# Optimization experiments

Hardware: AMD Instinct MI355X
Metric: run time of the kernel (lower is better)

Reference implementation:

```python
import jax, jax.numpy as jnp
import numpy as np

B, T, D, P, M = 4, 1024, 512, 64, 256


def setup_inputs() -> dict:
    key = jax.random.key(0)
    ks = jax.random.split(key, 10)
    s_d = 1.0 / np.sqrt(D)
    s_m = 1.0 / np.sqrt(M)
    s_p = 1.0 / np.sqrt(P)
    return {
        "inputs": jax.random.normal(ks[0], (B, T, D), dtype=jnp.float32),
        "ec": jax.random.normal(ks[1], (B, M), dtype=jnp.float32),
        "W1": jax.random.uniform(ks[2], (D, P), jnp.float32, -s_d, s_d),
        "b1": jax.random.uniform(ks[3], (P,), jnp.float32, -s_d, s_d),
        "W2": jax.random.uniform(ks[4], (D, P), jnp.float32, -s_d, s_d),
        "b2": jax.random.uniform(ks[5], (P,), jnp.float32, -s_d, s_d),
        "W3": jax.random.uniform(ks[6], (M, P), jnp.float32, -s_m, s_m),
        "b3": jax.random.uniform(ks[7], (P,), jnp.float32, -s_m, s_m),
        "wa_w": jax.random.uniform(ks[8], (P,), jnp.float32, -s_p, s_p),
        "wa_b": jax.random.uniform(ks[9], (), jnp.float32, -s_p, s_p),
    }


def reference(inputs, ec, W1, b1, W2, b2, W3, b3, wa_w, wa_b):
    # inputs: (B,T,D), ec: (B,M)
    w1h = inputs @ W1 + b1          # (B,T,P)
    w2h = inputs @ W2 + b2          # (B,T,P)
    w3e = ec @ W3 + b3              # (B,P)
    # Gt: (B,T,T,P) via broadcast add + tanh
    gt = jnp.tanh(w1h[:, :, None, :] + w2h[:, None, :, :] + w3e[:, None, None, :])
    at = jnp.einsum('btup,p->btu', gt, wa_w) + wa_b   # (B,T,T)
    at = jax.nn.softmax(at, axis=-1)
    out = jnp.einsum('btu,bud->btd', at, inputs)      # (B,T,D)
    return out
```

## Files before the change

kernel.cpp:

```cpp
#include <hip/hip_runtime.h>
#include <hip/hip_bf16.h>

constexpr int BB = 4;
constexpr int TT = 1024;
constexpr int DD = 512;
constexpr int PP = 64;
constexpr int MM = 256;

constexpr float CSCALE = 2.8853900817779268f;
constexpr float L2E = 1.4426950408889634f;

typedef __attribute__((ext_vector_type(8))) short v8s;
typedef __attribute__((ext_vector_type(4))) float v4f;

__device__ __forceinline__ unsigned short f2bf(float f) {
    unsigned u = __builtin_bit_cast(unsigned, f);
    unsigned r = (u + 0x7fffu + ((u >> 16) & 1u)) >> 16;
    return (unsigned short)r;
}

__global__ __launch_bounds__(256) void prep_kernel(
    const float* __restrict__ x, const float* __restrict__ ec,
    const float* __restrict__ W1, const float* __restrict__ b1,
    const float* __restrict__ W2, const float* __restrict__ b2,
    const float* __restrict__ W3, const float* __restrict__ b3,
    float* __restrict__ E1, float* __restrict__ E2, float* __restrict__ E3,
    unsigned short* __restrict__ xt) {
    __shared__ float tile[64][65];
    int bid = blockIdx.x;
    int tid = threadIdx.x;
    if (bid < 512) {
        int p = tid & 63;
        int rr = tid >> 6;
        int row0 = (bid << 3) + (rr << 1);
        const float* xr0 = x + (size_t)row0 * DD;
        const float* xr1 = xr0 + DD;
        float a10 = b1[p], a11 = b1[p];
        float a20 = b2[p], a21 = b2[p];
        #pragma unroll 4
        for (int d = 0; d < DD; d++) {
            float wv1 = W1[d * PP + p];
            float wv2 = W2[d * PP + p];
            float x0 = xr0[d];
            float x1 = xr1[d];
            a10 = fmaf(x0, wv1, a10);
            a11 = fmaf(x1, wv1, a11);
            a20 = fmaf(x0, wv2, a20);
            a21 = fmaf(x1, wv2, a21);
        }
        E1[(size_t)row0 * PP + p]       = __builtin_amdgcn_exp2f(a10 * CSCALE);
        E1[(size_t)(row0 + 1) * PP + p] = __builtin_amdgcn_exp2f(a11 * CSCALE);
        E2[(size_t)row0 * PP + p]       = __builtin_amdgcn_exp2f(a20 * CSCALE);
        E2[(size_t)(row0 + 1) * PP + p] = __builtin_amdgcn_exp2f(a21 * CSCALE);
    } else if (bid < 1024) {
        int q = bid - 512;
        int d0 = (q & 7) << 6;
        int u0 = ((q >> 3) & 15) << 6;
        int b = q >> 7;
        int c4 = (tid & 15) << 2, r = tid >> 4;
        #pragma unroll
        for (int i = 0; i < 4; i++) {
            int row = r + (i << 4);
            float4 v = *(const float4*)(x + ((size_t)b * TT + u0 + row) * DD + d0 + c4);
            tile[row][c4 + 0] = v.x;
            tile[row][c4 + 1] = v.y;
            tile[row][c4 + 2] = v.z;
            tile[row][c4 + 3] = v.w;
        }
        __syncthreads();
        int dd = tid >> 2;
        int uq = (tid & 3) << 4;
        unsigned short us[16];
        #pragma unroll
        for (int j = 0; j < 16; j++) us[j] = f2bf(tile[uq + j][dd]);
        uint4 w0, w1;
        w0.x = us[0] | ((unsigned)us[1] << 16);  w0.y = us[2] | ((unsigned)us[3] << 16);
        w0.z = us[4] | ((unsigned)us[5] << 16);  w0.w = us[6] | ((unsigned)us[7] << 16);
        w1.x = us[8] | ((unsigned)us[9] << 16);  w1.y = us[10] | ((unsigned)us[11] << 16);
        w1.z = us[12] | ((unsigned)us[13] << 16); w1.w = us[14] | ((unsigned)us[15] << 16);
        unsigned short* dst = xt + ((size_t)b * DD + d0 + dd) * TT + u0 + uq;
        *(uint4*)dst = w0;
        *(uint4*)(dst + 8) = w1;
    } else {
        int b = tid >> 6, p = tid & 63;
        float a = b3[p];
        const float* e = ec + (size_t)b * MM;
        #pragma unroll 4
        for (int m = 0; m < MM; m++) a = fmaf(e[m], W3[m * PP + p], a);
        E3[b * PP + p] = __builtin_amdgcn_exp2f(a * CSCALE);
    }
}

__global__ __launch_bounds__(256) void scores_kernel(
    const float* __restrict__ E1, const float* __restrict__ E2,
    const float* __restrict__ E3, const float* __restrict__ wa_w,
    const float* __restrict__ wa_b, unsigned short* __restrict__ at_bf) {
    __shared__ float sc_lds[32][256];
    __shared__ float sm[4][4];
    __shared__ float sl[4][4];
    int tid = threadIdx.x;
    int bid = blockIdx.x;
    int b = bid >> 8;
    int t0 = (bid & 255) << 2;
    int pp = tid & 7;
    int uu = tid >> 3;
    int p0 = pp << 3;
    int lane = tid & 63;
    int wv = tid >> 6;
    int my_i = pp & 3;

    float ww2[8], H[4][8];
    float base;
    {
        float4 wv0 = *(const float4*)(wa_w + p0);
        float4 wv1 = *(const float4*)(wa_w + p0 + 4);
        float s = wv0.x + wv0.y + wv0.z + wv0.w + wv1.x + wv1.y + wv1.z + wv1.w;
        s += __shfl_xor(s, 1, 64);
        s += __shfl_xor(s, 2, 64);
        s += __shfl_xor(s, 4, 64);
        base = (s + wa_b[0]) * L2E;
        ww2[0] = -2.f * L2E * wv0.x; ww2[1] = -2.f * L2E * wv0.y;
        ww2[2] = -2.f * L2E * wv0.z; ww2[3] = -2.f * L2E * wv0.w;
        ww2[4] = -2.f * L2E * wv1.x; ww2[5] = -2.f * L2E * wv1.y;
        ww2[6] = -2.f * L2E * wv1.z; ww2[7] = -2.f * L2E * wv1.w;
        float4 e3a = *(const float4*)(E3 + (b << 6) + p0);
        float4 e3b = *(const float4*)(E3 + (b << 6) + p0 + 4);
        #pragma unroll
        for (int i = 0; i < 4; i++) {
            const float* e1p = E1 + (((size_t)(b << 10) + t0 + i) << 6) + p0;
            float4 a = *(const float4*)e1p;
            float4 c = *(const float4*)(e1p + 4);
            H[i][0] = a.x * e3a.x; H[i][1] = a.y * e3a.y; H[i][2] = a.z * e3a.z; H[i][3] = a.w * e3a.w;
            H[i][4] = c.x * e3b.x; H[i][5] = c.y * e3b.y; H[i][6] = c.z * e3b.z; H[i][7] = c.w * e3b.w;
        }
    }

    float mown = -1e30f;
    for (int k = 0; k < 32; k++) {
        int u = (k << 5) + uu;
        const float* ep = E2 + (((size_t)(b << 10) + u) << 6) + p0;
        float4 e0 = *(const float4*)ep;
        float4 e1 = *(const float4*)(ep + 4);
        float ev[8] = {e0.x, e0.y, e0.z, e0.w, e1.x, e1.y, e1.z, e1.w};
        float own = 0.f;
        #pragma unroll
        for (int i = 0; i < 4; i++) {
            float a0 = 0.f, a1 = 0.f;
            #pragma unroll
            for (int j = 0; j < 8; j += 2) {
                a0 = fmaf(ww2[j],   __builtin_amdgcn_rcpf(fmaf(H[i][j],   ev[j],   1.0f)), a0);
                a1 = fmaf(ww2[j+1], __builtin_amdgcn_rcpf(fmaf(H[i][j+1], ev[j+1], 1.0f)), a1);
            }
            float s = a0 + a1;
            s += __shfl_xor(s, 1, 64);
            s += __shfl_xor(s, 2, 64);
            s += __shfl_xor(s, 4, 64);
            own = (my_i == i) ? s : own;
        }
        own += base;
        sc_lds[k][tid] = own;
        mown = fmaxf(mown, own);
    }
    mown = fmaxf(mown, __shfl_xor(mown, 4, 64));
    mown = fmaxf(mown, __shfl_xor(mown, 8, 64));
    mown = fmaxf(mown, __shfl_xor(mown, 16, 64));
    mown = fmaxf(mown, __shfl_xor(mown, 32, 64));
    if (lane < 4) sm[wv][lane] = mown;
    __syncthreads();
    float mx = fmaxf(fmaxf(sm[0][my_i], sm[1][my_i]), fmaxf(sm[2][my_i], sm[3][my_i]));

    float l = 0.f;
    for (int k = 0; k < 32; k++) {
        float s = sc_lds[k][tid];
        float e = __builtin_amdgcn_exp2f(s - mx);
        sc_lds[k][tid] = e;
        l += e;
    }
    l += __shfl_xor(l, 8, 64);
    l += __shfl_xor(l, 16, 64);
    l += __shfl_xor(l, 32, 64);
    if (lane < 4) sl[wv][lane] = l;
    __syncthreads();
    float inv = 1.0f / (sl[0][my_i] + sl[1][my_i] + sl[2][my_i] + sl[3][my_i]);

    if (pp < 4) {
        size_t rowbase = ((size_t)((b << 10) + t0 + my_i)) << 10;
        for (int k = 0; k < 32; k++) {
            float e = sc_lds[k][tid] * inv;
            at_bf[rowbase + (k << 5) + uu] = f2bf(e);
        }
    }
}

__global__ __launch_bounds__(256) void av_mfma_kernel(
    const unsigned short* __restrict__ at_bf, const unsigned short* __restrict__ xt,
    float* __restrict__ out) {
    __shared__ unsigned short As[64][72];
    __shared__ unsigned short Bs[64][72];
    int b = blockIdx.z;
    int m0 = blockIdx.y << 6;
    int n0 = blockIdx.x << 6;
    const unsigned short* A = at_bf + ((size_t)b << 20);
    const unsigned short* Bt = xt + (size_t)b * DD * TT;
    int tid = threadIdx.x;
    int lane = tid & 63;
    int wv = tid >> 6;
    int wm = (wv & 1) << 5;
    int wn = (wv >> 1) << 5;
    int l15 = lane & 15;
    int quad = lane >> 4;

    v4f acc00 = {0.f, 0.f, 0.f, 0.f}, acc01 = acc00, acc10 = acc00, acc11 = acc00;

    for (int k0 = 0; k0 < TT; k0 += 64) {
        __syncthreads();
        #pragma unroll
        for (int i = 0; i < 2; i++) {
            int s = (i << 8) + tid;
            int row = s >> 3, k8 = (s & 7) << 3;
            uint4 va = *(const uint4*)(A + (size_t)(m0 + row) * TT + k0 + k8);
            *(uint4*)&As[row][k8] = va;
            uint4 vb = *(const uint4*)(Bt + (size_t)(n0 + row) * TT + k0 + k8);
            *(uint4*)&Bs[row][k8] = vb;
        }
        __syncthreads();
        #pragma unroll
        for (int kq = 0; kq < 2; kq++) {
            int kc = (kq << 5) + (quad << 3);
            v8s a0 = *(const v8s*)&As[wm + l15][kc];
            v8s a1 = *(const v8s*)&As[wm + 16 + l15][kc];
            v8s b0 = *(const v8s*)&Bs[wn + l15][kc];
            v8s b1 = *(const v8s*)&Bs[wn + 16 + l15][kc];
            acc00 = __builtin_amdgcn_mfma_f32_16x16x32_bf16(a0, b0, acc00, 0, 0, 0);
            acc01 = __builtin_amdgcn_mfma_f32_16x16x32_bf16(a0, b1, acc01, 0, 0, 0);
            acc10 = __builtin_amdgcn_mfma_f32_16x16x32_bf16(a1, b0, acc10, 0, 0, 0);
            acc11 = __builtin_amdgcn_mfma_f32_16x16x32_bf16(a1, b1, acc11, 0, 0, 0);
        }
    }
    float* C = out + (size_t)b * TT * DD;
    int rbase = m0 + wm + (quad << 2);
    int cn = n0 + wn + l15;
    #pragma unroll
    for (int r = 0; r < 4; r++) {
        C[(size_t)(rbase + r) * DD + cn]           = acc00[r];
        C[(size_t)(rbase + r) * DD + cn + 16]      = acc01[r];
        C[(size_t)(rbase + 16 + r) * DD + cn]      = acc10[r];
        C[(size_t)(rbase + 16 + r) * DD + cn + 16] = acc11[r];
    }
}

extern "C" void kernel_launch(void* const* d_in, const int* in_sizes, int n_in,
                              void* d_out, int out_size, void* d_ws, size_t ws_size,
                              hipStream_t stream) {
    const float* inputs = (const float*)d_in[0];
    const float* ec     = (const float*)d_in[1];
    const float* W1     = (const float*)d_in[2];
    const float* b1     = (const float*)d_in[3];
    const float* W2     = (const float*)d_in[4];
    const float* b2     = (const float*)d_in[5];
    const float* W3     = (const float*)d_in[6];
    const float* b3     = (const float*)d_in[7];
    const float* wa_w   = (const float*)d_in[8];
    const float* wa_b   = (const float*)d_in[9];
    float* out = (float*)d_out;

    float* ws = (float*)d_ws;
    float* E1 = ws;
    float* E2 = ws + 262144;
    float* E3 = ws + 524288;
    unsigned short* at_bf = (unsigned short*)(ws + 524800);
    unsigned short* xt    = (unsigned short*)(ws + 524800 + 2097152);

    hipLaunchKernelGGL(prep_kernel, dim3(1025), dim3(256), 0, stream,
                       inputs, ec, W1, b1, W2, b2, W3, b3, E1, E2, E3, xt);
    hipLaunchKernelGGL(scores_kernel, dim3(1024), dim3(256), 0, stream,
                       E1, E2, E3, wa_w, wa_b, at_bf);
    hipLaunchKernelGGL(av_mfma_kernel, dim3(DD / 64, TT / 64, BB), dim3(256), 0, stream,
                       at_bf, xt, out);
}
```

Before: 174.5 us.

## Compute input projections with split-bf16 MFMA instead of scalar FMA loops

The scalar FP32 projection of inputs onto W1 and W2 in the prep kernel is replaced by a tiled MFMA GEMM. Each 64-row block stages X and the concatenated [W1|W2] through shared memory as hi/lo bf16 pairs and issues three bf16 MFMAs per tile to approximate FP32 accuracy. This cuts the prep grid from 1025 to 577 blocks and aims to remove the slow per-thread FMA loop. The costs are extra conversion work, more shared memory per block, and only 64 GEMM blocks, which may leave the GPU underoccupied.

```diff
diff --git a/kernel.cpp b/kernel.cpp
--- a/kernel.cpp
+++ b/kernel.cpp
@@ -17,6 +17,14 @@
     unsigned u = __builtin_bit_cast(unsigned, f);
     unsigned r = (u + 0x7fffu + ((u >> 16) & 1u)) >> 16;
     return (unsigned short)r;
+}
+__device__ __forceinline__ float bf2f(unsigned short h) {
+    return __builtin_bit_cast(float, (unsigned)h << 16);
+}
+__device__ __forceinline__ void split2(float v, unsigned short& h, unsigned short& l) {
+    unsigned short hh = f2bf(v);
+    h = hh;
+    l = f2bf(v - bf2f(hh));
 }
 
 __global__ __launch_bounds__(256) void prep_kernel(
@@ -26,34 +34,101 @@
     const float* __restrict__ W3, const float* __restrict__ b3,
     float* __restrict__ E1, float* __restrict__ E2, float* __restrict__ E3,
     unsigned short* __restrict__ xt) {
-    __shared__ float tile[64][65];
+    __shared__ unsigned short AsH[64][72];
+    __shared__ unsigned short AsL[64][72];
+    __shared__ unsigned short BsH[128][72];
+    __shared__ unsigned short BsL[128][72];
     int bid = blockIdx.x;
     int tid = threadIdx.x;
-    if (bid < 512) {
-        int p = tid & 63;
-        int rr = tid >> 6;
-        int row0 = (bid << 3) + (rr << 1);
-        const float* xr0 = x + (size_t)row0 * DD;
-        const float* xr1 = xr0 + DD;
-        float a10 = b1[p], a11 = b1[p];
-        float a20 = b2[p], a21 = b2[p];
-        #pragma unroll 4
-        for (int d = 0; d < DD; d++) {
-            float wv1 = W1[d * PP + p];
-            float wv2 = W2[d * PP + p];
-            float x0 = xr0[d];
-            float x1 = xr1[d];
-            a10 = fmaf(x0, wv1, a10);
-            a11 = fmaf(x1, wv1, a11);
-            a20 = fmaf(x0, wv2, a20);
-            a21 = fmaf(x1, wv2, a21);
-        }
-        E1[(size_t)row0 * PP + p]       = __builtin_amdgcn_exp2f(a10 * CSCALE);
-        E1[(size_t)(row0 + 1) * PP + p] = __builtin_amdgcn_exp2f(a11 * CSCALE);
-        E2[(size_t)row0 * PP + p]       = __builtin_amdgcn_exp2f(a20 * CSCALE);
-        E2[(size_t)(row0 + 1) * PP + p] = __builtin_amdgcn_exp2f(a21 * CSCALE);
-    } else if (bid < 1024) {
-        int q = bid - 512;
+
+    if (bid < 64) {
+        int m0 = bid << 6;
+        int lane = tid & 63;
+        int wv = tid >> 6;
+        int wm = (wv & 1) << 5;
+        int wn = (wv >> 1) << 6;
+        int l15 = lane & 15;
+        int quad = lane >> 4;
+
+        v4f acc[2][4];
+        #pragma unroll
+        for (int mt = 0; mt < 2; mt++)
+            #pragma unroll
+            for (int nt = 0; nt < 4; nt++) acc[mt][nt] = (v4f){0.f, 0.f, 0.f, 0.f};
+
+        for (int k0 = 0; k0 < DD; k0 += 64) {
+            __syncthreads();
+            #pragma unroll
+            for (int i = 0; i < 4; i++) {
+                int s = (i << 8) + tid;
+                int row = s >> 4, k4 = (s & 15) << 2;
+                float4 v = *(const float4*)(x + (size_t)(m0 + row) * DD + k0 + k4);
+                unsigned short h0, h1, h2, h3, l0, l1, l2, l3;
+                split2(v.x, h0, l0); split2(v.y, h1, l1);
+                split2(v.z, h2, l2); split2(v.w, h3, l3);
+                uint2 hw, lw;
+                hw.x = h0 | ((unsigned)h1 << 16); hw.y = h2 | ((unsigned)h3 << 16);
+                lw.x = l0 | ((unsigned)l1 << 16); lw.y = l2 | ((unsigned)l3 << 16);
+                *(uint2*)&AsH[row][k4] = hw;
+                *(uint2*)&AsL[row][k4] = lw;
+            }
+            #pragma unroll
+            for (int i = 0; i < 8; i++) {
+                int s = (i << 8) + tid;
+                int kk = s >> 5, n4 = (s & 31) << 2;
+                const float* src = (n4 < 64) ? (W1 + (size_t)(k0 + kk) * PP + n4)
+                                             : (W2 + (size_t)(k0 + kk) * PP + (n4 - 64));
+                float4 v = *(const float4*)src;
+                unsigned short h, l;
+                split2(v.x, h, l); BsH[n4 + 0][kk] = h; BsL[n4 + 0][kk] = l;
+                split2(v.y, h, l); BsH[n4 + 1][kk] = h; BsL[n4 + 1][kk] = l;
+                split2(v.z, h, l); BsH[n4 + 2][kk] = h; BsL[n4 + 2][kk] = l;
+                split2(v.w, h, l); BsH[n4 + 3][kk] = h; BsL[n4 + 3][kk] = l;
+            }
+            __syncthreads();
+            #pragma unroll
+            for (int kk = 0; kk < 64; kk += 32) {
+                int kc = kk + (quad << 3);
+                v8s aH[2], aL[2], bH[4], bL[4];
+                #pragma unroll
+                for (int mt = 0; mt < 2; mt++) {
+                    aH[mt] = *(const v8s*)&AsH[wm + (mt << 4) + l15][kc];
+                    aL[mt] = *(const v8s*)&AsL[wm + (mt << 4) + l15][kc];
+                }
+                #pragma unroll
+                for (int nt = 0; nt < 4; nt++) {
+                    bH[nt] = *(const v8s*)&BsH[wn + (nt << 4) + l15][kc];
+                    bL[nt] = *(const v8s*)&BsL[wn + (nt << 4) + l15][kc];
+                }
+                #pragma unroll
+                for (int mt = 0; mt < 2; mt++)
+                    #pragma unroll
+                    for (int nt = 0; nt < 4; nt++) {
+                        acc[mt][nt] = __builtin_amdgcn_mfma_f32_16x16x32_bf16(aH[mt], bH[nt], acc[mt][nt], 0, 0, 0);
+                        acc[mt][nt] = __builtin_amdgcn_mfma_f32_16x16x32_bf16(aH[mt], bL[nt], acc[mt][nt], 0, 0, 0);
+                        acc[mt][nt] = __builtin_amdgcn_mfma_f32_16x16x32_bf16(aL[mt], bH[nt], acc[mt][nt], 0, 0, 0);
+                    }
+            }
+        }
+        #pragma unroll
+        for (int nt = 0; nt < 4; nt++) {
+            int n = wn + (nt << 4) + l15;
+            int p = n & 63;
+            float bias = (n < 64) ? b1[p] : b2[p];
+            float* E = (n < 64) ? E1 : E2;
+            #pragma unroll
+            for (int mt = 0; mt < 2; mt++) {
+                int rbase = m0 + wm + (mt << 4) + (quad << 2);
+                #pragma unroll
+                for (int r = 0; r < 4; r++) {
+                    float h = acc[mt][nt][r] + bias;
+                    E[(size_t)(rbase + r) * PP + p] = __builtin_amdgcn_exp2f(h * CSCALE);
+                }
+            }
+        }
+    } else if (bid < 576) {
+        float (*tile)[65] = (float(*)[65])&AsH[0][0];
+        int q = bid - 64;
         int d0 = (q & 7) << 6;
         int u0 = ((q >> 3) & 15) << 6;
         int b = q >> 7;
@@ -271,7 +346,7 @@
     unsigned short* at_bf = (unsigned short*)(ws + 524800);
     unsigned short* xt    = (unsigned short*)(ws + 524800 + 2097152);
 
-    hipLaunchKernelGGL(prep_kernel, dim3(1025), dim3(256), 0, stream,
+    hipLaunchKernelGGL(prep_kernel, dim3(577), dim3(256), 0, stream,
                        inputs, ec, W1, b1, W2, b2, W3, b3, E1, E2, E3, xt);
     hipLaunchKernelGGL(scores_kernel, dim3(1024), dim3(256), 0, stream,
                        E1, E2, E3, wa_w, wa_b, at_bf);
```

Result: no change. 173.3 us (-0.7%).
